# Kernel tuning notes

Measured on AMD Instinct MI355X. Metric: run time of the kernel, lower is better.

The kernel has to match this reference:

```python
import jax, jax.numpy as jnp
import numpy as np

ALPHA = 0.9        # LIF membrane decay
THRESH = 1.0       # spike threshold
SURR_BETA = 4.0    # surrogate-gradient sharpness
TIME_STEPS = 32    # fabric simulation steps per token position


def _spike(v):
    """Heaviside spike with sigmoid surrogate gradient (straight-through)."""
    hard = (v >= THRESH).astype(v.dtype)
    soft = jax.nn.sigmoid(SURR_BETA * (v - THRESH))
    return soft + jax.lax.stop_gradient(hard - soft)


def setup_inputs() -> dict:
    key = jax.random.key(0)
    k0, k1, k2, k3 = jax.random.split(key, 4)
    B, S, D = 8, 128, 512
    N_in, N_out = 1024, 1024
    embeddings = jax.random.normal(k0, (B, S, D), jnp.float32)
    W_in = jax.random.normal(k1, (D, N_in), jnp.float32) / np.sqrt(D).astype(np.float32)
    b_in = jnp.zeros((N_in,), jnp.float32)
    W_conn = jax.random.normal(k2, (N_in, N_out), jnp.float32) / np.sqrt(N_in).astype(np.float32)
    W_out = jax.random.normal(k3, (N_out, D), jnp.float32) / np.sqrt(N_out).astype(np.float32)
    b_out = jnp.zeros((D,), jnp.float32)
    return {"embeddings": embeddings, "W_in": W_in, "b_in": b_in,
            "W_conn": W_conn, "W_out": W_out, "b_out": b_out}


def reference(embeddings, W_in, b_in, W_conn, W_out, b_out):
    B, S, D = embeddings.shape
    N_in = W_in.shape[1]
    N_out = W_conn.shape[1]

    # embed_to_snn + relu, precomputed for all positions: [B, S, N_in]
    snn_input = jax.nn.relu(jnp.einsum('bsd,dn->bsn', embeddings, W_in) + b_in)

    def time_step(carry, _):
        v_in, v_out, pos_input = carry
        # input population: leaky integrate external current
        v_in = ALPHA * v_in + pos_input
        s_in = _spike(v_in)
        v_in = v_in - s_in * THRESH          # soft reset
        # output population: driven by input-population spikes
        v_out = ALPHA * v_out + s_in @ W_conn
        s_out = _spike(v_out)
        v_out = v_out - s_out * THRESH
        n_spk = jax.lax.stop_gradient(s_in.sum() + s_out.sum())
        return (v_in, v_out, pos_input), (s_out, n_spk)

    def pos_step(carry, pos_input):
        v_in, v_out = carry
        (v_in, v_out, _), (s_outs, n_spks) = jax.lax.scan(
            time_step, (v_in, v_out, pos_input), None, length=TIME_STEPS)
        spike_acc = s_outs.sum(axis=0)       # [B, N_out], sum over timesteps
        pos_out = spike_acc @ W_out + b_out  # snn_to_embed
        return (v_in, v_out), (pos_out, n_spks.sum())

    v0_in = jnp.zeros((B, N_in), embeddings.dtype)
    v0_out = jnp.zeros((B, N_out), embeddings.dtype)
    snn_seq = jnp.swapaxes(snn_input, 0, 1)  # [S, B, N_in]: scan over positions
    _, (outs, spk_counts) = jax.lax.scan(pos_step, (v0_in, v0_out), snn_seq)

    output_embeddings = jnp.swapaxes(outs, 0, 1)  # [B, S, D]
    total_neurons = N_in + N_out
    spike_rate = spk_counts.sum() / (B * S * total_neurons * TIME_STEPS)
    return output_embeddings, spike_rate
```

## Files before the change

### kernel.cpp

```cpp
#include <hip/hip_runtime.h>
#include <stdint.h>

#define B 8
#define S 128
#define D 512
#define NIN 1024
#define NOUT 1024
#define T 32

typedef __attribute__((ext_vector_type(8))) short short8;
typedef __attribute__((ext_vector_type(4))) float floatx4;

__global__ __launch_bounds__(256) void k_gemm(const float* __restrict__ A,
                                              const float* __restrict__ Bm,
                                              const float* __restrict__ bias,
                                              float* __restrict__ C,
                                              int M, int N, int K, int relu)
{
    __shared__ float As[16][64];
    __shared__ float Bs[16][64];
    const int tid = threadIdx.x;
    const int bx = blockIdx.x, by = blockIdx.y;
    const int tx = tid & 15, ty = tid >> 4;
    const int ar = tid >> 2, ak = (tid & 3) << 2;
    const int bk = tid >> 4, bc = (tid & 15) << 2;
    float acc[4][4] = {{0.f,0.f,0.f,0.f},{0.f,0.f,0.f,0.f},
                       {0.f,0.f,0.f,0.f},{0.f,0.f,0.f,0.f}};
    for (int k0 = 0; k0 < K; k0 += 16) {
        float4 a4 = *(const float4*)(A + (size_t)(by*64 + ar)*K + k0 + ak);
        float4 b4 = *(const float4*)(Bm + (size_t)(k0 + bk)*N + bx*64 + bc);
        __syncthreads();
        As[ak+0][ar] = a4.x; As[ak+1][ar] = a4.y;
        As[ak+2][ar] = a4.z; As[ak+3][ar] = a4.w;
        *(float4*)&Bs[bk][bc] = b4;
        __syncthreads();
        #pragma unroll
        for (int kk = 0; kk < 16; ++kk) {
            float4 av = *(const float4*)&As[kk][ty << 2];
            float4 bv = *(const float4*)&Bs[kk][tx << 2];
            acc[0][0] = fmaf(av.x, bv.x, acc[0][0]);
            acc[0][1] = fmaf(av.x, bv.y, acc[0][1]);
            acc[0][2] = fmaf(av.x, bv.z, acc[0][2]);
            acc[0][3] = fmaf(av.x, bv.w, acc[0][3]);
            acc[1][0] = fmaf(av.y, bv.x, acc[1][0]);
            acc[1][1] = fmaf(av.y, bv.y, acc[1][1]);
            acc[1][2] = fmaf(av.y, bv.z, acc[1][2]);
            acc[1][3] = fmaf(av.y, bv.w, acc[1][3]);
            acc[2][0] = fmaf(av.z, bv.x, acc[2][0]);
            acc[2][1] = fmaf(av.z, bv.y, acc[2][1]);
            acc[2][2] = fmaf(av.z, bv.z, acc[2][2]);
            acc[2][3] = fmaf(av.z, bv.w, acc[2][3]);
            acc[3][0] = fmaf(av.w, bv.x, acc[3][0]);
            acc[3][1] = fmaf(av.w, bv.y, acc[3][1]);
            acc[3][2] = fmaf(av.w, bv.z, acc[3][2]);
            acc[3][3] = fmaf(av.w, bv.w, acc[3][3]);
        }
    }
    const int row0 = by*64 + (ty << 2), col0 = bx*64 + (tx << 2);
    float4 bb = *(const float4*)(bias + col0);
    #pragma unroll
    for (int i = 0; i < 4; ++i) {
        float4 o;
        o.x = acc[i][0] + bb.x; o.y = acc[i][1] + bb.y;
        o.z = acc[i][2] + bb.z; o.w = acc[i][3] + bb.w;
        if (relu) {
            o.x = fmaxf(o.x, 0.f); o.y = fmaxf(o.y, 0.f);
            o.z = fmaxf(o.z, 0.f); o.w = fmaxf(o.w, 0.f);
        }
        *(float4*)(C + (size_t)(row0 + i)*N + col0) = o;
    }
}

__global__ __launch_bounds__(256) void k_lif_inA(const float* __restrict__ snn,
                                                 unsigned int* __restrict__ sbits,
                                                 unsigned int* __restrict__ counters)
{
    const int tid = blockIdx.x * 256 + threadIdx.x;
    const int b = tid >> 10, n = tid & (NIN - 1);
    const float* cur = snn + (size_t)(b * S) * NIN + n;
    float v = 0.f;
    int cnt = 0;
    float I = cur[0];
    for (int s = 0; s < S; ++s) {
        const float In = (s + 1 < S) ? cur[(size_t)(s + 1) * NIN] : 0.f;
        unsigned int bits = 0u;
        #pragma unroll
        for (int t = 0; t < T; ++t) {
            v = __fadd_rn(__fmul_rn(0.9f, v), I);
            const bool sp = (v >= 1.0f);
            v = sp ? (v - 1.0f) : v;
            bits |= (sp ? 1u : 0u) << t;
        }
        sbits[(size_t)(b * S + s) * NIN + n] = bits;
        cnt += __popc(bits);
        I = In;
    }
    atomicAdd(counters, (unsigned int)cnt);
}

__global__ __launch_bounds__(256) void k_lif_inB(const unsigned int* __restrict__ sbits,
                                                 unsigned long long* __restrict__ masks)
{
    const int bs = blockIdx.x;
    const int w = threadIdx.x >> 6, lane = threadIdx.x & 63;
    #pragma unroll
    for (int i = 0; i < 4; ++i) {
        const int wq = w * 4 + i;
        const unsigned int bits = sbits[(size_t)bs * NIN + wq * 64 + lane];
        #pragma unroll
        for (int t = 0; t < T; ++t) {
            const unsigned long long m = __ballot((bits >> t) & 1u);
            if (lane == 0)
                masks[((size_t)bs * T + t) * 16 + wq] = m;
        }
    }
}

__global__ __launch_bounds__(256) void k_prep(const float* __restrict__ Wc,
                                              unsigned short* __restrict__ WhT,
                                              unsigned short* __restrict__ WlT)
{
    __shared__ float tile[64][65];
    const int k0 = blockIdx.x * 64, n0 = blockIdx.y * 64;
    const int tx = threadIdx.x & 63, ty = threadIdx.x >> 6;
    #pragma unroll
    for (int p = 0; p < 16; ++p) {
        const int kl = p*4 + ty;
        tile[kl][tx] = Wc[(size_t)(k0 + kl) * NOUT + n0 + tx];
    }
    __syncthreads();
    #pragma unroll
    for (int p = 0; p < 16; ++p) {
        const int nl = p*4 + ty;
        const float w = tile[tx][nl];
        const unsigned int u  = __float_as_uint(w);
        const unsigned int hb = (u + 0x7FFFu + ((u >> 16) & 1u)) & 0xFFFF0000u;
        const float hif = __uint_as_float(hb);
        const float lo  = w - hif;
        const unsigned int ul = __float_as_uint(lo);
        const unsigned short lob = (unsigned short)((ul + 0x7FFFu + ((ul >> 16) & 1u)) >> 16);
        WhT[(size_t)(n0 + nl) * NIN + k0 + tx] = (unsigned short)(hb >> 16);
        WlT[(size_t)(n0 + nl) * NIN + k0 + tx] = lob;
    }
}

__global__ __launch_bounds__(256) void k_conn_mfma(const uint4* __restrict__ masks128,
                                                   const unsigned short* __restrict__ WhT,
                                                   const unsigned short* __restrict__ WlT,
                                                   float* __restrict__ Iout,
                                                   int s0, int P)
{
    __shared__ uint4 lut[256];
    __shared__ unsigned short Bsm[2][64][136];

    const int tid = threadIdx.x;
    {
        const unsigned int bb = (unsigned int)tid;
        unsigned int r[4];
        #pragma unroll
        for (int i = 0; i < 4; ++i) {
            const unsigned int b0 = (bb >> (2*i)) & 1u, b1 = (bb >> (2*i+1)) & 1u;
            r[i] = (b0 ? 0x3F80u : 0u) | (b1 ? 0x3F800000u : 0u);
        }
        lut[tid] = make_uint4(r[0], r[1], r[2], r[3]);
    }

    const int w = tid >> 6, lane = tid & 63;
    const int r16 = lane & 15, q = lane >> 4;
    const int PT = P * T;
    const int rowblk = blockIdx.x * 256 + w * 64;
    const int cb = blockIdx.y * 64;

    const uint4* aptr[4];
    #pragma unroll
    for (int f = 0; f < 4; ++f) {
        const int r = rowblk + f*16 + r16;
        const int b = r / PT;
        const int within = r - b * PT;
        const int grow = (b * S + s0) * T + within;
        aptr[f] = masks128 + (size_t)grow * 8;
    }

    const int sflat0 = tid;
    floatx4 acc[4][4];
    #pragma unroll
    for (int f = 0; f < 4; ++f)
        #pragma unroll
        for (int c = 0; c < 4; ++c)
            acc[f][c] = (floatx4){0.f, 0.f, 0.f, 0.f};

    for (int ch = 0; ch < 8; ++ch) {
        __syncthreads();
        #pragma unroll
        for (int i = 0; i < 8; ++i) {
            const int flat = sflat0 + i * 256;
            const int mat  = flat >> 10;
            const int rest = flat & 1023;
            const int col  = rest >> 4;
            const int k16  = rest & 15;
            const unsigned short* src =
                (mat ? WlT : WhT) + (size_t)(cb + col) * NIN + ch * 128 + k16 * 8;
            *(uint4*)&Bsm[mat][col][k16 * 8] = *(const uint4*)src;
        }
        uint4 aw[4];
        #pragma unroll
        for (int f = 0; f < 4; ++f) aw[f] = aptr[f][ch];
        __syncthreads();

        #pragma unroll
        for (int kc = 0; kc < 4; ++kc) {
            short8 bh[4], bl[4];
            #pragma unroll
            for (int c = 0; c < 4; ++c) {
                bh[c] = *(const short8*)&Bsm[0][c*16 + r16][kc*32 + q*8];
                bl[c] = *(const short8*)&Bsm[1][c*16 + r16][kc*32 + q*8];
            }
            #pragma unroll
            for (int f = 0; f < 4; ++f) {
                const unsigned int word = (kc == 0) ? aw[f].x : (kc == 1) ? aw[f].y
                                         : (kc == 2) ? aw[f].z : aw[f].w;
                const unsigned int byte = (word >> (q * 8)) & 0xFFu;
                const short8 a = *(const short8*)&lut[byte];
                #pragma unroll
                for (int c = 0; c < 4; ++c) {
                    acc[f][c] = __builtin_amdgcn_mfma_f32_16x16x32_bf16(a, bh[c], acc[f][c], 0, 0, 0);
                    acc[f][c] = __builtin_amdgcn_mfma_f32_16x16x32_bf16(a, bl[c], acc[f][c], 0, 0, 0);
                }
            }
        }
    }

    #pragma unroll
    for (int f = 0; f < 4; ++f) {
        const int row = rowblk + f*16 + q*4;
        #pragma unroll
        for (int c = 0; c < 4; ++c) {
            const int col = cb + c*16 + r16;
            #pragma unroll
            for (int i = 0; i < 4; ++i)
                Iout[(size_t)(row + i) * NOUT + col] = acc[f][c][i];
        }
    }
}

__global__ __launch_bounds__(256) void k_lif_out(const float* __restrict__ Iout,
                                                 float* __restrict__ vstate,
                                                 float* __restrict__ sacc_out,
                                                 unsigned int* __restrict__ counters,
                                                 int s0, int P, int init)
{
    const int tid = blockIdx.x * 256 + threadIdx.x;
    const int b = tid >> 10, n = tid & (NOUT - 1);
    const int Tc = P * T;
    float v = init ? 0.f : vstate[tid];
    const float* ip = Iout + (size_t)b * Tc * NOUT + n;
    int cnt = 0;

    float cur[T];
    #pragma unroll
    for (int t = 0; t < T; ++t) cur[t] = ip[(size_t)t * NOUT];

    for (int sl = 0; sl < P; ++sl) {
        float nxt[T];
        const bool has = (sl + 1 < P);
        if (has) {
            const float* ip2 = ip + (size_t)(sl + 1) * T * NOUT;
            #pragma unroll
            for (int t = 0; t < T; ++t) nxt[t] = ip2[(size_t)t * NOUT];
        }
        float sacc = 0.f;
        #pragma unroll
        for (int t = 0; t < T; ++t) {
            v = __fadd_rn(__fmul_rn(0.9f, v), cur[t]);
            const bool sp = (v >= 1.0f);
            v = sp ? (v - 1.0f) : v;
            sacc += sp ? 1.f : 0.f;
            cnt += sp ? 1 : 0;
        }
        sacc_out[(size_t)(b*S + s0 + sl) * NOUT + n] = sacc;
        if (has) {
            #pragma unroll
            for (int t = 0; t < T; ++t) cur[t] = nxt[t];
        }
    }
    vstate[tid] = v;
    atomicAdd(counters + 1, (unsigned int)cnt);
}

__global__ void k_init(unsigned int* c)
{
    if (threadIdx.x < 2) c[threadIdx.x] = 0u;
}

__global__ void k_rate(const unsigned int* __restrict__ c, float* __restrict__ out)
{
    if (threadIdx.x == 0 && blockIdx.x == 0) {
        const float total = (float)c[0] + (float)c[1];
        out[0] = total / (float)(B * S * (NIN + NOUT) * T);
    }
}

extern "C" void kernel_launch(void* const* d_in, const int* in_sizes, int n_in,
                              void* d_out, int out_size, void* d_ws, size_t ws_size,
                              hipStream_t stream)
{
    const float* E    = (const float*)d_in[0];
    const float* Win  = (const float*)d_in[1];
    const float* bin  = (const float*)d_in[2];
    const float* Wc   = (const float*)d_in[3];
    const float* Wout = (const float*)d_in[4];
    const float* bout = (const float*)d_in[5];
    float* out = (float*)d_out;

    char* w = (char*)d_ws;
    float* snn              = (float*)(w);
    unsigned short* WhT     = (unsigned short*)(w);
    unsigned short* WlT     = (unsigned short*)(w + (2 << 20));
    unsigned long long* msk = (unsigned long long*)(w + (4 << 20));
    float* sacc             = (float*)(w + (8 << 20));
    unsigned int* sbits     = (unsigned int*)(w + (8 << 20));
    float* vst              = (float*)(w + (12 << 20));
    unsigned int* cnt       = (unsigned int*)(w + (12 << 20) + (64 << 10));
    float* Iout             = (float*)(w + (13 << 20));

    const size_t base = (size_t)13 << 20;
    const size_t avail = (ws_size > base) ? (ws_size - base) : 0;
    int P = 1;
    if      (avail >= (size_t)B * 128 * T * NOUT * 4) P = 128;
    else if (avail >= (size_t)B *  16 * T * NOUT * 4) P = 16;
    else if (avail >= (size_t)B *   4 * T * NOUT * 4) P = 4;

    k_init<<<1, 64, 0, stream>>>(cnt);

    dim3 g1(NIN / 64, (B * S) / 64);
    k_gemm<<<g1, 256, 0, stream>>>(E, Win, bin, snn, B * S, NIN, D, 1);

    k_lif_inA<<<32, 256, 0, stream>>>(snn, sbits, cnt);
    k_lif_inB<<<B * S, 256, 0, stream>>>(sbits, msk);

    dim3 gp(NIN / 64, NOUT / 64);
    k_prep<<<gp, 256, 0, stream>>>(Wc, WhT, WlT);

    for (int c = 0; c < S / P; ++c) {
        dim3 gc((B * P * T) / 256, NOUT / 64);
        k_conn_mfma<<<gc, 256, 0, stream>>>((const uint4*)msk, WhT, WlT, Iout, c * P, P);
        k_lif_out<<<32, 256, 0, stream>>>(Iout, vst, sacc, cnt, c * P, P, c == 0 ? 1 : 0);
    }

    dim3 g2(D / 64, (B * S) / 64);
    k_gemm<<<g2, 256, 0, stream>>>(sacc, Wout, bout, out, B * S, D, NOUT, 0);

    k_rate<<<1, 64, 0, stream>>>(cnt, out + (size_t)B * S * D);
}
```

Measured before the change: 473.4 us.

## Spread LIF scans over more blocks, deepen prefetch, and rework MFMA B-tile staging

The two sequential LIF scan kernels now run as 128 blocks of 64 threads instead of 32 blocks of 256, spreading the serial recurrence over more compute units. Their input prefetch now runs several positions ahead, four for the input layer and two for the output layer. The connection MFMA kernel stores the B tile in LDS pre-arranged in MFMA fragment order, with source pointers computed once outside the chunk loop. It also drops the shared-memory LUT and builds the bf16 spike operand in registers from the mask bits. These changes target latency in the serial scans and LDS traffic in the GEMM, at the cost of more registers and ALU work per thread.

```diff
diff --git a/kernel.cpp b/kernel.cpp
--- a/kernel.cpp
+++ b/kernel.cpp
@@ -71,29 +71,42 @@
     }
 }
 
-__global__ __launch_bounds__(256) void k_lif_inA(const float* __restrict__ snn,
-                                                 unsigned int* __restrict__ sbits,
-                                                 unsigned int* __restrict__ counters)
-{
-    const int tid = blockIdx.x * 256 + threadIdx.x;
+__global__ __launch_bounds__(64) void k_lif_inA(const float* __restrict__ snn,
+                                                unsigned int* __restrict__ sbits,
+                                                unsigned int* __restrict__ counters)
+{
+    const int tid = blockIdx.x * 64 + threadIdx.x;
     const int b = tid >> 10, n = tid & (NIN - 1);
     const float* cur = snn + (size_t)(b * S) * NIN + n;
     float v = 0.f;
     int cnt = 0;
-    float I = cur[0];
-    for (int s = 0; s < S; ++s) {
-        const float In = (s + 1 < S) ? cur[(size_t)(s + 1) * NIN] : 0.f;
-        unsigned int bits = 0u;
-        #pragma unroll
-        for (int t = 0; t < T; ++t) {
-            v = __fadd_rn(__fmul_rn(0.9f, v), I);
-            const bool sp = (v >= 1.0f);
-            v = sp ? (v - 1.0f) : v;
-            bits |= (sp ? 1u : 0u) << t;
-        }
-        sbits[(size_t)(b * S + s) * NIN + n] = bits;
-        cnt += __popc(bits);
-        I = In;
+    float I[4];
+    #pragma unroll
+    for (int j = 0; j < 4; ++j) I[j] = cur[(size_t)j * NIN];
+    for (int s = 0; s < S; s += 4) {
+        float In[4];
+        if (s + 4 < S) {
+            #pragma unroll
+            for (int j = 0; j < 4; ++j) In[j] = cur[(size_t)(s + 4 + j) * NIN];
+        } else {
+            #pragma unroll
+            for (int j = 0; j < 4; ++j) In[j] = 0.f;
+        }
+        #pragma unroll
+        for (int j = 0; j < 4; ++j) {
+            unsigned int bits = 0u;
+            #pragma unroll
+            for (int t = 0; t < T; ++t) {
+                v = __fadd_rn(__fmul_rn(0.9f, v), I[j]);
+                const bool sp = (v >= 1.0f);
+                v = sp ? (v - 1.0f) : v;
+                bits |= (sp ? 1u : 0u) << t;
+            }
+            sbits[(size_t)(b * S + s + j) * NIN + n] = bits;
+            cnt += __popc(bits);
+        }
+        #pragma unroll
+        for (int j = 0; j < 4; ++j) I[j] = In[j];
     }
     atomicAdd(counters, (unsigned int)cnt);
 }
@@ -150,21 +163,9 @@
                                                    float* __restrict__ Iout,
                                                    int s0, int P)
 {
-    __shared__ uint4 lut[256];
-    __shared__ unsigned short Bsm[2][64][136];
+    __shared__ unsigned short Bsm[2 * 4 * 4 * 64 * 8];
 
     const int tid = threadIdx.x;
-    {
-        const unsigned int bb = (unsigned int)tid;
-        unsigned int r[4];
-        #pragma unroll
-        for (int i = 0; i < 4; ++i) {
-            const unsigned int b0 = (bb >> (2*i)) & 1u, b1 = (bb >> (2*i+1)) & 1u;
-            r[i] = (b0 ? 0x3F80u : 0u) | (b1 ? 0x3F800000u : 0u);
-        }
-        lut[tid] = make_uint4(r[0], r[1], r[2], r[3]);
-    }
-
     const int w = tid >> 6, lane = tid & 63;
     const int r16 = lane & 15, q = lane >> 4;
     const int PT = P * T;
@@ -181,7 +182,18 @@
         aptr[f] = masks128 + (size_t)grow * 8;
     }
 
-    const int sflat0 = tid;
+    const unsigned short* sptr[8];
+    #pragma unroll
+    for (int i = 0; i < 8; ++i) {
+        const int f = tid + i * 256;
+        const int lane_s = f & 63;
+        const int slot = f >> 6;
+        const int c = slot & 3, kc = (slot >> 2) & 3, mat = slot >> 4;
+        sptr[i] = (mat ? WlT : WhT)
+                + (size_t)(cb + c*16 + (lane_s & 15)) * NIN
+                + kc * 32 + (lane_s >> 4) * 8;
+    }
+
     floatx4 acc[4][4];
     #pragma unroll
     for (int f = 0; f < 4; ++f)
@@ -189,19 +201,14 @@
         for (int c = 0; c < 4; ++c)
             acc[f][c] = (floatx4){0.f, 0.f, 0.f, 0.f};
 
+    const unsigned short* bp = Bsm + (size_t)lane * 8;
+
     for (int ch = 0; ch < 8; ++ch) {
         __syncthreads();
         #pragma unroll
-        for (int i = 0; i < 8; ++i) {
-            const int flat = sflat0 + i * 256;
-            const int mat  = flat >> 10;
-            const int rest = flat & 1023;
-            const int col  = rest >> 4;
-            const int k16  = rest & 15;
-            const unsigned short* src =
-                (mat ? WlT : WhT) + (size_t)(cb + col) * NIN + ch * 128 + k16 * 8;
-            *(uint4*)&Bsm[mat][col][k16 * 8] = *(const uint4*)src;
-        }
+        for (int i = 0; i < 8; ++i)
+            *(uint4*)(Bsm + (size_t)(tid + i * 256) * 8) =
+                *(const uint4*)(sptr[i] + ch * 128);
         uint4 aw[4];
         #pragma unroll
         for (int f = 0; f < 4; ++f) aw[f] = aptr[f][ch];
@@ -212,15 +219,20 @@
             short8 bh[4], bl[4];
             #pragma unroll
             for (int c = 0; c < 4; ++c) {
-                bh[c] = *(const short8*)&Bsm[0][c*16 + r16][kc*32 + q*8];
-                bl[c] = *(const short8*)&Bsm[1][c*16 + r16][kc*32 + q*8];
+                bh[c] = *(const short8*)(bp + (( kc*4 + c) << 9));
+                bl[c] = *(const short8*)(bp + ((16 + kc*4 + c) << 9));
             }
             #pragma unroll
             for (int f = 0; f < 4; ++f) {
                 const unsigned int word = (kc == 0) ? aw[f].x : (kc == 1) ? aw[f].y
                                          : (kc == 2) ? aw[f].z : aw[f].w;
                 const unsigned int byte = (word >> (q * 8)) & 0xFFu;
-                const short8 a = *(const short8*)&lut[byte];
+                union { unsigned int u[4]; short8 s; } A;
+                #pragma unroll
+                for (int j = 0; j < 4; ++j)
+                    A.u[j] = (((byte >> (2*j)) & 1u) ? 0x3F80u : 0u)
+                           | (((byte >> (2*j+1)) & 1u) ? 0x3F800000u : 0u);
+                const short8 a = A.s;
                 #pragma unroll
                 for (int c = 0; c < 4; ++c) {
                     acc[f][c] = __builtin_amdgcn_mfma_f32_16x16x32_bf16(a, bh[c], acc[f][c], 0, 0, 0);
@@ -243,45 +255,57 @@
     }
 }
 
-__global__ __launch_bounds__(256) void k_lif_out(const float* __restrict__ Iout,
-                                                 float* __restrict__ vstate,
-                                                 float* __restrict__ sacc_out,
-                                                 unsigned int* __restrict__ counters,
-                                                 int s0, int P, int init)
-{
-    const int tid = blockIdx.x * 256 + threadIdx.x;
+__global__ __launch_bounds__(64) void k_lif_out(const float* __restrict__ Iout,
+                                                float* __restrict__ vstate,
+                                                float* __restrict__ sacc_out,
+                                                unsigned int* __restrict__ counters,
+                                                int s0, int P, int init)
+{
+    const int tid = blockIdx.x * 64 + threadIdx.x;
     const int b = tid >> 10, n = tid & (NOUT - 1);
     const int Tc = P * T;
     float v = init ? 0.f : vstate[tid];
     const float* ip = Iout + (size_t)b * Tc * NOUT + n;
     int cnt = 0;
 
-    float cur[T];
-    #pragma unroll
-    for (int t = 0; t < T; ++t) cur[t] = ip[(size_t)t * NOUT];
-
-    for (int sl = 0; sl < P; ++sl) {
-        float nxt[T];
-        const bool has = (sl + 1 < P);
-        if (has) {
-            const float* ip2 = ip + (size_t)(sl + 1) * T * NOUT;
-            #pragma unroll
-            for (int t = 0; t < T; ++t) nxt[t] = ip2[(size_t)t * NOUT];
-        }
-        float sacc = 0.f;
-        #pragma unroll
-        for (int t = 0; t < T; ++t) {
-            v = __fadd_rn(__fmul_rn(0.9f, v), cur[t]);
-            const bool sp = (v >= 1.0f);
-            v = sp ? (v - 1.0f) : v;
-            sacc += sp ? 1.f : 0.f;
-            cnt += sp ? 1 : 0;
-        }
-        sacc_out[(size_t)(b*S + s0 + sl) * NOUT + n] = sacc;
-        if (has) {
-            #pragma unroll
-            for (int t = 0; t < T; ++t) cur[t] = nxt[t];
-        }
+    float cur[2][T];
+    #pragma unroll
+    for (int t = 0; t < T; ++t) cur[0][t] = ip[(size_t)t * NOUT];
+    if (P > 1) {
+        const float* p1 = ip + (size_t)T * NOUT;
+        #pragma unroll
+        for (int t = 0; t < T; ++t) cur[1][t] = p1[(size_t)t * NOUT];
+    }
+
+    for (int sl = 0; sl < P; sl += 2) {
+        float nxt[2][T];
+        #pragma unroll
+        for (int g = 0; g < 2; ++g) {
+            if (sl + 2 + g < P) {
+                const float* p2 = ip + (size_t)(sl + 2 + g) * T * NOUT;
+                #pragma unroll
+                for (int t = 0; t < T; ++t) nxt[g][t] = p2[(size_t)t * NOUT];
+            }
+        }
+        #pragma unroll
+        for (int g = 0; g < 2; ++g) {
+            if (sl + g < P) {
+                float sacc = 0.f;
+                #pragma unroll
+                for (int t = 0; t < T; ++t) {
+                    v = __fadd_rn(__fmul_rn(0.9f, v), cur[g][t]);
+                    const bool sp = (v >= 1.0f);
+                    v = sp ? (v - 1.0f) : v;
+                    sacc += sp ? 1.f : 0.f;
+                    cnt += sp ? 1 : 0;
+                }
+                sacc_out[(size_t)(b*S + s0 + sl + g) * NOUT + n] = sacc;
+            }
+        }
+        #pragma unroll
+        for (int g = 0; g < 2; ++g)
+            #pragma unroll
+            for (int t = 0; t < T; ++t) cur[g][t] = nxt[g][t];
     }
     vstate[tid] = v;
     atomicAdd(counters + 1, (unsigned int)cnt);
@@ -335,7 +359,7 @@
     dim3 g1(NIN / 64, (B * S) / 64);
     k_gemm<<<g1, 256, 0, stream>>>(E, Win, bin, snn, B * S, NIN, D, 1);
 
-    k_lif_inA<<<32, 256, 0, stream>>>(snn, sbits, cnt);
+    k_lif_inA<<<128, 64, 0, stream>>>(snn, sbits, cnt);
     k_lif_inB<<<B * S, 256, 0, stream>>>(sbits, msk);
 
     dim3 gp(NIN / 64, NOUT / 64);
@@ -344,7 +368,7 @@
     for (int c = 0; c < S / P; ++c) {
         dim3 gc((B * P * T) / 256, NOUT / 64);
         k_conn_mfma<<<gc, 256, 0, stream>>>((const uint4*)msk, WhT, WlT, Iout, c * P, P);
-        k_lif_out<<<32, 256, 0, stream>>>(Iout, vst, sacc, cnt, c * P, P, c == 0 ? 1 : 0);
+        k_lif_out<<<128, 64, 0, stream>>>(Iout, vst, sacc, cnt, c * P, P, c == 0 ? 1 : 0);
     }
 
     dim3 g2(D / 64, (B * S) / 64);
```

Result: slower. 495.9 us (+4.8%).
